# Kernel tuning notes

Hardware: AMD Instinct MI355X
Metric: run time of the kernel (lower is better)

Reference implementation:

```python
import jax, jax.numpy as jnp
import numpy as np

N_NODES = 10000


def _add_self_loops(edge_index, n):
    loops = jnp.arange(n, dtype=edge_index.dtype)
    row = jnp.concatenate([edge_index[0], loops])
    col = jnp.concatenate([edge_index[1], loops])
    return row, col


def _gcn_norm(row, col, n):
    # symmetric normalization: deg^-1/2[row] * deg^-1/2[col], deg counted on col
    deg = jax.ops.segment_sum(jnp.ones_like(col, dtype=jnp.float32), col, num_segments=n)
    dis = jnp.where(deg > 0, jax.lax.rsqrt(jnp.maximum(deg, 1.0)), 0.0)
    return dis[row] * dis[col]


def _gcn_conv(x, W, b, row, col, norm, n):
    h = x @ W                      # [N, out]
    m = h[row] * norm[:, None]     # [E+N, out] gathered, normalized messages
    out = jax.ops.segment_sum(m, col, num_segments=n)
    return out + b


def setup_inputs() -> dict:
    key = jax.random.key(0)
    ks = jax.random.split(key, 10)
    N, E, Cin, Cout = N_NODES, 160000, 256, 512
    x = jax.random.normal(ks[0], (N, Cin), dtype=jnp.float32)
    edge_index = jax.random.randint(ks[1], (2, E), 0, N, dtype=jnp.int64)
    s = 1.0 / np.sqrt(Cin)
    s2 = 1.0 / np.sqrt(Cout)
    return {
        "x": x,
        "edge_index": edge_index,
        "W1": jax.random.normal(ks[2], (Cin, Cout), dtype=jnp.float32) * s,
        "b1": jnp.zeros((Cout,), dtype=jnp.float32),
        "W2": jax.random.normal(ks[3], (Cout, Cout), dtype=jnp.float32) * s2,
        "b2": jnp.zeros((Cout,), dtype=jnp.float32),
        "W3": jax.random.normal(ks[4], (Cout, Cout), dtype=jnp.float32) * s2,
        "b3": jnp.zeros((Cout,), dtype=jnp.float32),
        "W4": jax.random.normal(ks[5], (Cout, Cout), dtype=jnp.float32) * s2,
        "b4": jnp.zeros((Cout,), dtype=jnp.float32),
    }


def reference(x, edge_index, W1, b1, W2, b2, W3, b3, W4, b4):
    n = x.shape[0]
    row, col = _add_self_loops(edge_index, n)
    norm = _gcn_norm(row, col, n)
    h = jax.nn.relu(_gcn_conv(x, W1, b1, row, col, norm, n))
    h = jax.nn.relu(_gcn_conv(h, W2, b2, row, col, norm, n))
    h = jax.nn.relu(_gcn_conv(h, W3, b3, row, col, norm, n))
    h = _gcn_conv(h, W4, b4, row, col, norm, n)
    return h.reshape(-1, 5, h.shape[-1])  # [N/5, 5, 512]
```

## Files before the change

kernel.cpp:

```cpp
#include <hip/hip_runtime.h>
#include <hip/hip_bf16.h>

#define N_NODES 10000
#define N_EDGES 160000

typedef __hip_bfloat16 bf16;
typedef unsigned short u16;
typedef float f32x4 __attribute__((ext_vector_type(4)));
typedef short s16x8 __attribute__((ext_vector_type(8)));
typedef unsigned short us8 __attribute__((ext_vector_type(8)));
typedef unsigned short us4 __attribute__((ext_vector_type(4)));

static __device__ __forceinline__ float b2f(u16 u) {
    unsigned v = (unsigned)u << 16;
    return __uint_as_float(v);
}
static __device__ __forceinline__ u16 f2b(float f) {
    bf16 b = __float2bfloat16(f);
    return *reinterpret_cast<u16*>(&b);
}

#define GLDS(gp, lp)                                                         \
    __builtin_amdgcn_global_load_lds(                                        \
        (const __attribute__((address_space(1))) void*)(const void*)(gp),    \
        (__attribute__((address_space(3))) void*)(lp), 16, 0, 0)

template <int CE> struct VecSel;
template <> struct VecSel<4> { typedef us4 T; };
template <> struct VecSel<8> { typedef us8 T; };


__global__ void k_prep0(const int* __restrict__ ei,
                        int* __restrict__ row, int* __restrict__ col,
                        int* __restrict__ deg) {
    bool is64 = true;
#pragma unroll
    for (int i = 0; i < 8; ++i) is64 = is64 && (ei[2 * i + 1] == 0);
    int t = blockIdx.x * 256 + threadIdx.x;
    if (t < N_NODES) deg[t] = 0;
    if (t < N_EDGES) {
        if (is64) {
            row[t] = ei[2 * t];
            col[t] = ei[2 * (N_EDGES + t)];
        } else {
            row[t] = ei[t];
            col[t] = ei[N_EDGES + t];
        }
    }
}

__global__ void k_count(const int* __restrict__ col, int* deg) {
    int e = blockIdx.x * 256 + threadIdx.x;
    if (e < N_EDGES) atomicAdd(&deg[col[e]], 1);
}

__global__ void k_scan_all(const int* __restrict__ deg, float* __restrict__ dis,
                           int* __restrict__ off, int* __restrict__ cur) {
    __shared__ int sums[256];
    int t = threadIdx.x;
    const int seg = (N_NODES + 255) >> 8;
    int lo = t * seg, hi = lo + seg;
    if (lo > N_NODES) lo = N_NODES;
    if (hi > N_NODES) hi = N_NODES;
    int s = 0;
    for (int i = lo; i < hi; ++i) {
        dis[i] = rsqrtf((float)deg[i] + 1.0f);
        s += deg[i];
    }
    sums[t] = s;
    __syncthreads();
    for (int d = 1; d < 256; d <<= 1) {
        int v = (t >= d) ? sums[t - d] : 0;
        __syncthreads();
        sums[t] += v;
        __syncthreads();
    }
    int run = sums[t] - s;
    for (int i = lo; i < hi; ++i) {
        off[i] = run;
        cur[i] = run;
        run += deg[i];
    }
    if (t == 255) off[N_NODES] = sums[255];
}

__global__ void k_fill(const int* __restrict__ row, const int* __restrict__ col,
                       const float* __restrict__ dis, int* cur,
                       int* __restrict__ crow, float* __restrict__ cnorm) {
    int e = blockIdx.x * 256 + threadIdx.x;
    if (e < N_EDGES) {
        int r = row[e], c = col[e];
        int p = atomicAdd(&cur[c], 1);
        crow[p] = r;
        cnorm[p] = dis[r] * dis[c];
    }
}

__global__ void k_convx(const float* __restrict__ x, u16* __restrict__ xb) {
    int i = blockIdx.x * 256 + threadIdx.x;
    float4 v = *(const float4*)(x + (size_t)i * 4);
    us4 st;
    st[0] = f2b(v.x); st[1] = f2b(v.y); st[2] = f2b(v.z); st[3] = f2b(v.w);
    *(us4*)(xb + (size_t)i * 4) = st;
}

__global__ void k_transpose(const float* __restrict__ W1, const float* __restrict__ W2,
                            const float* __restrict__ W3, const float* __restrict__ W4,
                            u16* __restrict__ T1, u16* __restrict__ T2,
                            u16* __restrict__ T3, u16* __restrict__ T4) {
    __shared__ u16 tile[32][33];
    int z = blockIdx.z;
    const float* W = (z == 0) ? W1 : (z == 1) ? W2 : (z == 2) ? W3 : W4;
    u16* WT        = (z == 0) ? T1 : (z == 1) ? T2 : (z == 2) ? T3 : T4;
    int K = (z == 0) ? 256 : 512;
    int k0 = blockIdx.y * 32;
    if (k0 >= K) return;
    int n0 = blockIdx.x * 32;
    int tx = threadIdx.x, ty = threadIdx.y;
    for (int i = 0; i < 32; i += 8)
        tile[ty + i][tx] = f2b(W[(size_t)(k0 + ty + i) * 512 + n0 + tx]);
    __syncthreads();
    for (int i = 0; i < 32; i += 8)
        WT[(size_t)(n0 + ty + i) * K + k0 + tx] = tile[tx][ty + i];
}


template <int C, int NCH>
__global__ void k_agg(const u16* __restrict__ in, u16* __restrict__ out,
                      const int* __restrict__ off, const int* __restrict__ crow,
                      const float* __restrict__ cnorm, const float* __restrict__ dis) {
    const int CE = C / (64 * NCH);
    typedef typename VecSel<CE>::T VT;
    int wid = blockIdx.x * 4 + (threadIdx.x >> 6);
    int lane = threadIdx.x & 63;
    int node = wid / NCH;
    if (node >= N_NODES) return;
    int ch = wid % NCH;
    int c = ch * (CE * 64) + lane * CE;

    float d = dis[node];
    VT sv = *(const VT*)(in + (size_t)node * C + c);
    float a0[CE], a1[CE], a2[CE], a3[CE];
#pragma unroll
    for (int j = 0; j < CE; ++j) {
        a0[j] = b2f(sv[j]) * d * d;
        a1[j] = 0.f; a2[j] = 0.f; a3[j] = 0.f;
    }

    int b = off[node], e = off[node + 1];
    int i = b;
    for (; i + 3 < e; i += 4) {
        int r0 = crow[i], r1 = crow[i + 1], r2 = crow[i + 2], r3 = crow[i + 3];
        float n0 = cnorm[i], n1 = cnorm[i + 1], n2 = cnorm[i + 2], n3 = cnorm[i + 3];
        VT v0 = *(const VT*)(in + (size_t)r0 * C + c);
        VT v1 = *(const VT*)(in + (size_t)r1 * C + c);
        VT v2 = *(const VT*)(in + (size_t)r2 * C + c);
        VT v3 = *(const VT*)(in + (size_t)r3 * C + c);
#pragma unroll
        for (int j = 0; j < CE; ++j) {
            a0[j] = fmaf(b2f(v0[j]), n0, a0[j]);
            a1[j] = fmaf(b2f(v1[j]), n1, a1[j]);
            a2[j] = fmaf(b2f(v2[j]), n2, a2[j]);
            a3[j] = fmaf(b2f(v3[j]), n3, a3[j]);
        }
    }
    for (; i < e; ++i) {
        int r0 = crow[i];
        float n0 = cnorm[i];
        VT v0 = *(const VT*)(in + (size_t)r0 * C + c);
#pragma unroll
        for (int j = 0; j < CE; ++j) a0[j] = fmaf(b2f(v0[j]), n0, a0[j]);
    }
    VT st;
#pragma unroll
    for (int j = 0; j < CE; ++j) st[j] = f2b((a0[j] + a1[j]) + (a2[j] + a3[j]));
    *(VT*)(out + (size_t)node * C + c) = st;
}


static __device__ __forceinline__ void st_out(float* out, size_t idx, float v) { out[idx] = v; }
static __device__ __forceinline__ void st_out(u16* out, size_t idx, float v) { out[idx] = f2b(v); }

template <typename OT>
__global__ __launch_bounds__(256) void k_gemm(
        const u16* __restrict__ A, const u16* __restrict__ BT,
        const float* __restrict__ bias, OT* __restrict__ out,
        int M, int K, int NO, int relu) {
    __shared__ u16 As[4][64][32];
    __shared__ u16 Bs[4][64][32];

    int tid = threadIdx.x;
    int w = tid >> 6;
    int lane = tid & 63;
    int wm = w >> 1, wn = w & 1;
    int m0 = blockIdx.x * 64;
    int n0 = blockIdx.y * 64;
    int l15 = lane & 15;
    int kq = lane >> 4;

    int srow = lane >> 2;
    int skc  = (lane & 3) * 8;
    const u16* agp[4];
    const u16* bgp[4];
    u16* al[4];
    u16* bl[4];
#pragma unroll
    for (int j = 0; j < 4; ++j) {
        int arw = m0 + j * 16 + srow; if (arw > M - 1) arw = M - 1;
        agp[j] = A + (size_t)arw * K + w * 32 + skc;
        bgp[j] = BT + (size_t)(n0 + j * 16 + srow) * K + w * 32 + skc;
        al[j] = &As[w][j * 16][0];
        bl[j] = &Bs[w][j * 16][0];
    }

    int aRow0 = wm * 32 + l15, aRow1 = aRow0 + 16;
    int bRow0 = wn * 32 + l15, bRow1 = bRow0 + 16;

    f32x4 acc00 = {0.f, 0.f, 0.f, 0.f};
    f32x4 acc01 = acc00, acc10 = acc00, acc11 = acc00;

    for (int k0 = 0; k0 < K; k0 += 128) {
#pragma unroll
        for (int j = 0; j < 4; ++j) GLDS(agp[j] + k0, al[j]);
#pragma unroll
        for (int j = 0; j < 4; ++j) GLDS(bgp[j] + k0, bl[j]);
        __syncthreads();
#pragma unroll
        for (int p = 0; p < 4; ++p) {
            s16x8 a0 = *(const s16x8*)&As[p][aRow0][kq * 8];
            s16x8 a1 = *(const s16x8*)&As[p][aRow1][kq * 8];
            s16x8 b0 = *(const s16x8*)&Bs[p][bRow0][kq * 8];
            s16x8 b1 = *(const s16x8*)&Bs[p][bRow1][kq * 8];
            acc00 = __builtin_amdgcn_mfma_f32_16x16x32_bf16(a0, b0, acc00, 0, 0, 0);
            acc01 = __builtin_amdgcn_mfma_f32_16x16x32_bf16(a0, b1, acc01, 0, 0, 0);
            acc10 = __builtin_amdgcn_mfma_f32_16x16x32_bf16(a1, b0, acc10, 0, 0, 0);
            acc11 = __builtin_amdgcn_mfma_f32_16x16x32_bf16(a1, b1, acc11, 0, 0, 0);
        }
        __syncthreads();
    }

    int r0 = (lane >> 4) * 4;
    int cm0 = m0 + wm * 32;
    int cn0 = n0 + wn * 32;
    float bv0 = bias[cn0 + l15];
    float bv1 = bias[cn0 + 16 + l15];
#pragma unroll
    for (int r = 0; r < 4; ++r) {
        int rowa = cm0 + r0 + r;
        if (rowa < M) {
            float v = acc00[r] + bv0;
            if (relu) v = fmaxf(v, 0.f);
            st_out(out, (size_t)rowa * NO + cn0 + l15, v);
            v = acc01[r] + bv1;
            if (relu) v = fmaxf(v, 0.f);
            st_out(out, (size_t)rowa * NO + cn0 + 16 + l15, v);
        }
        int rowb = rowa + 16;
        if (rowb < M) {
            float v = acc10[r] + bv0;
            if (relu) v = fmaxf(v, 0.f);
            st_out(out, (size_t)rowb * NO + cn0 + l15, v);
            v = acc11[r] + bv1;
            if (relu) v = fmaxf(v, 0.f);
            st_out(out, (size_t)rowb * NO + cn0 + 16 + l15, v);
        }
    }
}


extern "C" void kernel_launch(void* const* d_in, const int* in_sizes, int n_in,
                              void* d_out, int out_size, void* d_ws, size_t ws_size,
                              hipStream_t stream) {
    const float* x  = (const float*)d_in[0];
    const int*   ei = (const int*)d_in[1];
    const float* W1 = (const float*)d_in[2];
    const float* b1 = (const float*)d_in[3];
    const float* W2 = (const float*)d_in[4];
    const float* b2 = (const float*)d_in[5];
    const float* W3 = (const float*)d_in[6];
    const float* b3 = (const float*)d_in[7];
    const float* W4 = (const float*)d_in[8];
    const float* b4 = (const float*)d_in[9];

    char* ws = (char*)d_ws;
    size_t o = 0;
    auto alloc = [&](size_t bytes) {
        char* p = ws + o;
        o = (o + bytes + 255) & ~(size_t)255;
        return p;
    };
    int*   row   = (int*)alloc(N_EDGES * 4);
    int*   col   = (int*)alloc(N_EDGES * 4);
    int*   deg   = (int*)alloc(N_NODES * 4);
    float* dis   = (float*)alloc(N_NODES * 4);
    int*   off   = (int*)alloc((N_NODES + 1) * 4);
    int*   cur   = (int*)alloc(N_NODES * 4);
    int*   crow  = (int*)alloc(N_EDGES * 4);
    float* cnorm = (float*)alloc(N_EDGES * 4);
    u16*   WT1   = (u16*)alloc((size_t)512 * 256 * 2);
    u16*   WT2   = (u16*)alloc((size_t)512 * 512 * 2);
    u16*   WT3   = (u16*)alloc((size_t)512 * 512 * 2);
    u16*   WT4   = (u16*)alloc((size_t)512 * 512 * 2);
    u16*   xb    = (u16*)alloc((size_t)N_NODES * 256 * 2);
    u16*   s     = (u16*)alloc((size_t)N_NODES * 512 * 2);
    u16*   h     = (u16*)alloc((size_t)N_NODES * 512 * 2);
    float* outb  = (float*)d_out;

    dim3 b256(256);
    const int gE = (N_EDGES + 255) / 256;
    const dim3 gG(157, 8);
    const int gA1 = (N_NODES + 3) / 4;
    const int gA2 = (N_NODES * 2 + 3) / 4;

    k_prep0<<<gE, b256, 0, stream>>>(ei, row, col, deg);
    k_count<<<gE, b256, 0, stream>>>(col, deg);
    k_scan_all<<<1, b256, 0, stream>>>(deg, dis, off, cur);
    k_fill<<<gE, b256, 0, stream>>>(row, col, dis, cur, crow, cnorm);
    k_convx<<<N_NODES * 256 / 4 / 256, b256, 0, stream>>>(x, xb);
    k_transpose<<<dim3(16, 16, 4), dim3(32, 8), 0, stream>>>(W1, W2, W3, W4,
                                                             WT1, WT2, WT3, WT4);

    k_agg<256, 1><<<gA1, b256, 0, stream>>>(xb, s, off, crow, cnorm, dis);
    k_gemm<u16><<<gG, b256, 0, stream>>>(s, WT1, b1, h, N_NODES, 256, 512, 1);
    k_agg<512, 2><<<gA2, b256, 0, stream>>>(h, s, off, crow, cnorm, dis);
    k_gemm<u16><<<gG, b256, 0, stream>>>(s, WT2, b2, h, N_NODES, 512, 512, 1);
    k_agg<512, 2><<<gA2, b256, 0, stream>>>(h, s, off, crow, cnorm, dis);
    k_gemm<u16><<<gG, b256, 0, stream>>>(s, WT3, b3, h, N_NODES, 512, 512, 1);
    k_agg<512, 2><<<gA2, b256, 0, stream>>>(h, s, off, crow, cnorm, dis);
    k_gemm<float><<<gG, b256, 0, stream>>>(s, WT4, b4, outb, N_NODES, 512, 512, 0);
}
```

Baseline: 300.7 us.

## Double-buffer GEMM K loop, one wave per node in aggregation, fuse x conversion

The GEMM moves from a single 128-wide K stage to double-buffered 64-wide stages. The next tile's global-to-LDS loads are issued before the MFMAs on the current tile, and one barrier per iteration is dropped. The aggregation kernel now uses one wave per node with 8-element vectors for 512 channels instead of splitting channels across two waves, which halves the number of edge-index and norm reads. The x fp32-to-bf16 conversion is merged into the prep kernel to save a launch. Risks include higher register pressure in aggregation, fewer waves for latency hiding, and a possible hazard in buffer reuse without a trailing barrier.

```diff
diff --git a/kernel.cpp b/kernel.cpp
--- a/kernel.cpp
+++ b/kernel.cpp
@@ -32,7 +32,8 @@
 
 __global__ void k_prep0(const int* __restrict__ ei,
                         int* __restrict__ row, int* __restrict__ col,
-                        int* __restrict__ deg) {
+                        int* __restrict__ deg,
+                        const float* __restrict__ x, u16* __restrict__ xb) {
     bool is64 = true;
 #pragma unroll
     for (int i = 0; i < 8; ++i) is64 = is64 && (ei[2 * i + 1] == 0);
@@ -46,6 +47,12 @@
             row[t] = ei[t];
             col[t] = ei[N_EDGES + t];
         }
+    }
+    if (t < N_NODES * 256 / 4) {
+        float4 v = *(const float4*)(x + (size_t)t * 4);
+        us4 st;
+        st[0] = f2b(v.x); st[1] = f2b(v.y); st[2] = f2b(v.z); st[3] = f2b(v.w);
+        *(us4*)(xb + (size_t)t * 4) = st;
     }
 }
 
@@ -94,14 +101,6 @@
         crow[p] = r;
         cnorm[p] = dis[r] * dis[c];
     }
-}
-
-__global__ void k_convx(const float* __restrict__ x, u16* __restrict__ xb) {
-    int i = blockIdx.x * 256 + threadIdx.x;
-    float4 v = *(const float4*)(x + (size_t)i * 4);
-    us4 st;
-    st[0] = f2b(v.x); st[1] = f2b(v.y); st[2] = f2b(v.z); st[3] = f2b(v.w);
-    *(us4*)(xb + (size_t)i * 4) = st;
 }
 
 __global__ void k_transpose(const float* __restrict__ W1, const float* __restrict__ W2,
@@ -125,18 +124,16 @@
 }
 
 
-template <int C, int NCH>
+template <int C>
 __global__ void k_agg(const u16* __restrict__ in, u16* __restrict__ out,
                       const int* __restrict__ off, const int* __restrict__ crow,
                       const float* __restrict__ cnorm, const float* __restrict__ dis) {
-    const int CE = C / (64 * NCH);
+    const int CE = C / 64;
     typedef typename VecSel<CE>::T VT;
-    int wid = blockIdx.x * 4 + (threadIdx.x >> 6);
+    int node = blockIdx.x * 4 + (threadIdx.x >> 6);
     int lane = threadIdx.x & 63;
-    int node = wid / NCH;
     if (node >= N_NODES) return;
-    int ch = wid % NCH;
-    int c = ch * (CE * 64) + lane * CE;
+    int c = lane * CE;
 
     float d = dis[node];
     VT sv = *(const VT*)(in + (size_t)node * C + c);
@@ -186,8 +183,8 @@
         const u16* __restrict__ A, const u16* __restrict__ BT,
         const float* __restrict__ bias, OT* __restrict__ out,
         int M, int K, int NO, int relu) {
-    __shared__ u16 As[4][64][32];
-    __shared__ u16 Bs[4][64][32];
+    __shared__ u16 As[2][2][64][32];
+    __shared__ u16 Bs[2][2][64][32];
 
     int tid = threadIdx.x;
     int w = tid >> 6;
@@ -198,20 +195,17 @@
     int l15 = lane & 15;
     int kq = lane >> 4;
 
+    int sp  = w & 1;
+    int srb = (w >> 1) * 32;
     int srow = lane >> 2;
     int skc  = (lane & 3) * 8;
-    const u16* agp[4];
-    const u16* bgp[4];
-    u16* al[4];
-    u16* bl[4];
-#pragma unroll
-    for (int j = 0; j < 4; ++j) {
-        int arw = m0 + j * 16 + srow; if (arw > M - 1) arw = M - 1;
-        agp[j] = A + (size_t)arw * K + w * 32 + skc;
-        bgp[j] = BT + (size_t)(n0 + j * 16 + srow) * K + w * 32 + skc;
-        al[j] = &As[w][j * 16][0];
-        bl[j] = &Bs[w][j * 16][0];
-    }
+
+    int ar0 = m0 + srb + srow;      if (ar0 > M - 1) ar0 = M - 1;
+    int ar1 = m0 + srb + 16 + srow; if (ar1 > M - 1) ar1 = M - 1;
+    const u16* agp0 = A + (size_t)ar0 * K + sp * 32 + skc;
+    const u16* agp1 = A + (size_t)ar1 * K + sp * 32 + skc;
+    const u16* bgp0 = BT + (size_t)(n0 + srb + srow) * K + sp * 32 + skc;
+    const u16* bgp1 = BT + (size_t)(n0 + srb + 16 + srow) * K + sp * 32 + skc;
 
     int aRow0 = wm * 32 + l15, aRow1 = aRow0 + 16;
     int bRow0 = wn * 32 + l15, bRow1 = bRow0 + 16;
@@ -219,24 +213,33 @@
     f32x4 acc00 = {0.f, 0.f, 0.f, 0.f};
     f32x4 acc01 = acc00, acc10 = acc00, acc11 = acc00;
 
-    for (int k0 = 0; k0 < K; k0 += 128) {
-#pragma unroll
-        for (int j = 0; j < 4; ++j) GLDS(agp[j] + k0, al[j]);
-#pragma unroll
-        for (int j = 0; j < 4; ++j) GLDS(bgp[j] + k0, bl[j]);
+    GLDS(agp0, &As[0][sp][srb][0]);
+    GLDS(agp1, &As[0][sp][srb + 16][0]);
+    GLDS(bgp0, &Bs[0][sp][srb][0]);
+    GLDS(bgp1, &Bs[0][sp][srb + 16][0]);
+
+    int nIter = K >> 6;
+    for (int it = 0; it < nIter; ++it) {
         __syncthreads();
-#pragma unroll
-        for (int p = 0; p < 4; ++p) {
-            s16x8 a0 = *(const s16x8*)&As[p][aRow0][kq * 8];
-            s16x8 a1 = *(const s16x8*)&As[p][aRow1][kq * 8];
-            s16x8 b0 = *(const s16x8*)&Bs[p][bRow0][kq * 8];
-            s16x8 b1 = *(const s16x8*)&Bs[p][bRow1][kq * 8];
+        int cb = it & 1, nb = cb ^ 1;
+        if (it + 1 < nIter) {
+            int kn = (it + 1) << 6;
+            GLDS(agp0 + kn, &As[nb][sp][srb][0]);
+            GLDS(agp1 + kn, &As[nb][sp][srb + 16][0]);
+            GLDS(bgp0 + kn, &Bs[nb][sp][srb][0]);
+            GLDS(bgp1 + kn, &Bs[nb][sp][srb + 16][0]);
+        }
+#pragma unroll
+        for (int p = 0; p < 2; ++p) {
+            s16x8 a0 = *(const s16x8*)&As[cb][p][aRow0][kq * 8];
+            s16x8 a1 = *(const s16x8*)&As[cb][p][aRow1][kq * 8];
+            s16x8 b0 = *(const s16x8*)&Bs[cb][p][bRow0][kq * 8];
+            s16x8 b1 = *(const s16x8*)&Bs[cb][p][bRow1][kq * 8];
             acc00 = __builtin_amdgcn_mfma_f32_16x16x32_bf16(a0, b0, acc00, 0, 0, 0);
             acc01 = __builtin_amdgcn_mfma_f32_16x16x32_bf16(a0, b1, acc01, 0, 0, 0);
             acc10 = __builtin_amdgcn_mfma_f32_16x16x32_bf16(a1, b0, acc10, 0, 0, 0);
             acc11 = __builtin_amdgcn_mfma_f32_16x16x32_bf16(a1, b1, acc11, 0, 0, 0);
         }
-        __syncthreads();
     }
 
     int r0 = (lane >> 4) * 4;
@@ -308,24 +311,23 @@
 
     dim3 b256(256);
     const int gE = (N_EDGES + 255) / 256;
+    const int gP = (N_NODES * 256 / 4 + 255) / 256;
     const dim3 gG(157, 8);
-    const int gA1 = (N_NODES + 3) / 4;
-    const int gA2 = (N_NODES * 2 + 3) / 4;
-
-    k_prep0<<<gE, b256, 0, stream>>>(ei, row, col, deg);
+    const int gA = (N_NODES + 3) / 4;
+
+    k_prep0<<<gP, b256, 0, stream>>>(ei, row, col, deg, x, xb);
     k_count<<<gE, b256, 0, stream>>>(col, deg);
     k_scan_all<<<1, b256, 0, stream>>>(deg, dis, off, cur);
     k_fill<<<gE, b256, 0, stream>>>(row, col, dis, cur, crow, cnorm);
-    k_convx<<<N_NODES * 256 / 4 / 256, b256, 0, stream>>>(x, xb);
     k_transpose<<<dim3(16, 16, 4), dim3(32, 8), 0, stream>>>(W1, W2, W3, W4,
                                                              WT1, WT2, WT3, WT4);
 
-    k_agg<256, 1><<<gA1, b256, 0, stream>>>(xb, s, off, crow, cnorm, dis);
+    k_agg<256><<<gA, b256, 0, stream>>>(xb, s, off, crow, cnorm, dis);
     k_gemm<u16><<<gG, b256, 0, stream>>>(s, WT1, b1, h, N_NODES, 256, 512, 1);
-    k_agg<512, 2><<<gA2, b256, 0, stream>>>(h, s, off, crow, cnorm, dis);
+    k_agg<512><<<gA, b256, 0, stream>>>(h, s, off, crow, cnorm, dis);
     k_gemm<u16><<<gG, b256, 0, stream>>>(s, WT2, b2, h, N_NODES, 512, 512, 1);
-    k_agg<512, 2><<<gA2, b256, 0, stream>>>(h, s, off, crow, cnorm, dis);
+    k_agg<512><<<gA, b256, 0, stream>>>(h, s, off, crow, cnorm, dis);
     k_gemm<u16><<<gG, b256, 0, stream>>>(s, WT3, b3, h, N_NODES, 512, 512, 1);
-    k_agg<512, 2><<<gA2, b256, 0, stream>>>(h, s, off, crow, cnorm, dis);
+    k_agg<512><<<gA, b256, 0, stream>>>(h, s, off, crow, cnorm, dis);
     k_gemm<float><<<gG, b256, 0, stream>>>(s, WT4, b4, outb, N_NODES, 512, 512, 0);
 }
```

New measurement: 296.5 us. About the same (-1.4%).
